# Kernel optimization log

Measured on AMD Instinct MI355X. Metric: run time of the kernel, lower is better.

Reference implementation:

```python
import jax, jax.numpy as jnp
import numpy as np

KSIZE, STRIDES, D_NEURON, DK, DV, NH, DACT, FINAL_DIM = 4, 2, 128, 128, 256, 8, 8, 256
N = KSIZE * KSIZE          # 16 neurons per window
DKH = DK // NH             # 16 == N (required by broadcast in original code)
DVH = DV // NH             # 32


def setup_inputs() -> dict:
    key = jax.random.key(0)
    ks = jax.random.split(key, 12)
    B, H, W, C = 32, 64, 64, 256
    def dense(kw, kb, fan_in, fan_out):
        w = jax.random.normal(kw, (fan_in, fan_out), jnp.float32) / np.sqrt(fan_in)
        b = jnp.zeros((fan_out,), jnp.float32)
        return w, b
    inps = jax.random.normal(ks[0], (B, H, W, C), jnp.float32)
    neuron_emb = jax.random.normal(ks[1], (KSIZE, KSIZE, D_NEURON), jnp.float32) / np.sqrt(D_NEURON)
    wkq_w, wkq_b = dense(ks[2], ks[3], D_NEURON, 2 * DK)
    wv_w, wv_b = dense(ks[4], ks[5], C, DV)
    wgactq_w, wgactq_b = dense(ks[6], ks[7], D_NEURON, DACT)
    wgactk_w, wgactk_b = dense(ks[8], ks[9], C, DACT)
    wf_w, wf_b = dense(ks[10], ks[11], DV, FINAL_DIM)
    return dict(inps=inps, neuron_emb=neuron_emb, wkq_w=wkq_w, wkq_b=wkq_b,
                wv_w=wv_w, wv_b=wv_b, wgactq_w=wgactq_w, wgactq_b=wgactq_b,
                wgactk_w=wgactk_w, wgactk_b=wgactk_b, wf_w=wf_w, wf_b=wf_b)


def _forward(inps, neuron_emb, wkq_w, wkq_b, wv_w, wv_b,
             wgactq_w, wgactq_b, wgactk_w, wgactk_b, wf_w, wf_b):
    B, H, W, C = inps.shape
    # ---- neural structures (tiny, per-head n x n softmax) ----
    kq = neuron_emb @ wkq_w + wkq_b                      # (k,k,2dk)
    k_part, q_part = jnp.split(kq, 2, axis=-1)           # each (k,k,dk)
    flat = lambda t: t.reshape(N, NH, DKH).transpose(1, 0, 2)   # (Nh,n,dkh)
    fk, fq = flat(k_part), flat(q_part)
    # broadcast add requires dkh == n: logits[h,i,j] = fq[h,i,j] + fk[h,j,i]
    logits = fq + fk.transpose(0, 2, 1)                  # (Nh,n,n)
    structures = jax.nn.softmax(logits, axis=-1)
    s0 = structures[:, 0, :]                             # (Nh,n) row 0 per head
    # ---- activation amounts (dacth == 1, i.e. dact == Nh) ----
    actk = inps @ wgactk_w + wgactk_b                    # (B,H,W,Nh)
    actq = (neuron_emb @ wgactq_w + wgactq_b).reshape(N, NH)   # (n,Nh)
    qv = actq[N - 2]                                     # slice [-2:-1] -> (Nh,)
    g = jax.nn.relu(qv[None, None, None, :] + actk)      # (B,H,W,Nh)
    denom = jnp.sum(g, axis=(1, 2), keepdims=True)       # (B,1,1,Nh)
    act = (float(H * W) / (denom + 1e-6)) * g            # (B,H,W,Nh)
    # ---- values, gated per head ----
    v = inps @ wv_w + wv_b                               # (B,H,W,dv)
    v = (v.reshape(B, H, W, NH, DVH) * act[..., None]).reshape(B, H, W, DV)
    # ---- SAME-padded im2col patches (TF extract_patches ordering kh,kw,c) ----
    nH, nW = -(-H // STRIDES), -(-W // STRIDES)
    pad_h = max((nH - 1) * STRIDES + KSIZE - H, 0)
    pad_w = max((nW - 1) * STRIDES + KSIZE - W, 0)
    vp = jnp.pad(v, ((0, 0), (pad_h // 2, pad_h - pad_h // 2),
                     (pad_w // 2, pad_w - pad_w // 2), (0, 0)))
    hi = (nH - 1) * STRIDES + 1
    wi = (nW - 1) * STRIDES + 1
    patches = jnp.stack([vp[:, i:i + hi:STRIDES, j:j + wi:STRIDES, :]
                         for i in range(KSIZE) for j in range(KSIZE)],
                        axis=3)                           # (B,nH,nW,n,dv)
    p = patches.reshape(B, nH, nW, N, NH, DVH)
    # weighted reduce over window positions with structure row 0
    out = jnp.einsum('hn,bxynhd->bxyhd', s0, p).reshape(B, nH, nW, DV)
    return out @ wf_w + wf_b                             # (B,nH,nW,final_dim)


def reference(inps, neuron_emb, wkq_w, wkq_b, wv_w, wv_b,
              wgactq_w, wgactq_b, wgactk_w, wgactk_b, wf_w, wf_b):
    return _forward(inps, neuron_emb, wkq_w, wkq_b, wv_w, wv_b,
                    wgactq_w, wgactq_b, wgactk_w, wgactk_b, wf_w, wf_b)
```

## Files before the change

### kernel.cpp

```cpp
#include <hip/hip_runtime.h>
#include <hip/hip_bf16.h>

#define B_    32
#define H_    64
#define W_    64
#define C_    256
#define NH_   8
#define N_    16
#define PIX_  (B_*H_*W_)
#define OUTPIX_ (B_*32*32)

typedef __hip_bfloat16 bf16;
typedef __attribute__((ext_vector_type(8))) short bf16x8;
typedef __attribute__((ext_vector_type(4))) float f32x4;

__device__ __forceinline__ float bf2f(unsigned short u) {
  union { unsigned int i; float f; } v; v.i = ((unsigned int)u) << 16; return v.f;
}
__device__ __forceinline__ unsigned pk2(float a, float b) {
  union { __hip_bfloat162 h2; unsigned u; } c;
  c.h2 = __float22bfloat162_rn(make_float2(a, b));
  return c.u;
}
__device__ __forceinline__ bf16x8 cvt8(float4 lo, float4 hi) {
  union { bf16x8 v; unsigned u[4]; } r;
  r.u[0] = pk2(lo.x, lo.y); r.u[1] = pk2(lo.z, lo.w);
  r.u[2] = pk2(hi.x, hi.y); r.u[3] = pk2(hi.z, hi.w);
  return r.v;
}

__global__ __launch_bounds__(256) void k1_setup(
    const float* __restrict__ emb, const float* __restrict__ wkq_w,
    const float* __restrict__ wkq_b, const float* __restrict__ wgq_w,
    const float* __restrict__ wgq_b,
    float* __restrict__ s0, float* __restrict__ qv) {
  __shared__ float lq[128];
  __shared__ float lk[16][8];
  int t = threadIdx.x;
  if (t < 128) {
    float acc = wkq_b[128 + t];
    for (int e = 0; e < 128; ++e) acc += emb[e] * wkq_w[e * 256 + 128 + t];
    lq[t] = acc;
  } else {
    int idx = t - 128; int j = idx >> 3, h = idx & 7;
    float acc = wkq_b[h * 16];
    for (int e = 0; e < 128; ++e) acc += emb[j * 128 + e] * wkq_w[e * 256 + h * 16];
    lk[j][h] = acc;
  }
  __syncthreads();
  if (t < 8) {
    float l[16]; float m = -1e30f;
    for (int j = 0; j < 16; ++j) { l[j] = lq[t * 16 + j] + lk[j][t]; m = fmaxf(m, l[j]); }
    float s = 0.f;
    for (int j = 0; j < 16; ++j) { l[j] = expf(l[j] - m); s += l[j]; }
    float inv = 1.f / s;
    for (int j = 0; j < 16; ++j) s0[t * 16 + j] = l[j] * inv;
    float acc = wgq_b[t];
    for (int e = 0; e < 128; ++e) acc += emb[14 * 128 + e] * wgq_w[e * 8 + t];
    qv[t] = acc;
  }
}

__global__ __launch_bounds__(256) void prep(
    const float* __restrict__ wv, const float* __restrict__ wf,
    const float* __restrict__ wgk,
    bf16* __restrict__ wvT, bf16* __restrict__ wfT, bf16* __restrict__ wgkT) {
  int bid = blockIdx.x, t = threadIdx.x;
  if (bid < 32) {
    __shared__ unsigned short tile[64][72];
    const float* src = (bid < 16) ? wv : wf;
    bf16* dst = (bid < 16) ? wvT : wfT;
    int tb = bid & 15, tr = tb >> 2, tc = tb & 3;
#pragma unroll
    for (int it = 0; it < 16; ++it) {
      int idx = it * 256 + t, row = idx >> 6, col = idx & 63;
      bf16 h = __float2bfloat16(src[(tr * 64 + row) * 256 + tc * 64 + col]);
      tile[row][col] = *(unsigned short*)&h;
    }
    __syncthreads();
#pragma unroll
    for (int it = 0; it < 16; ++it) {
      int idx = it * 256 + t, row = idx >> 6, col = idx & 63;
      dst[(tc * 64 + row) * 256 + (tr * 64 + col)] = *(bf16*)&tile[col][row];
    }
  } else {
    __shared__ float g[2048];
#pragma unroll
    for (int it = 0; it < 8; ++it) g[it * 256 + t] = wgk[it * 256 + t];
    __syncthreads();
#pragma unroll
    for (int it = 0; it < 16; ++it) {
      int idx = it * 256 + t, a = idx >> 8, k = idx & 255;
      float v = (a < 8) ? g[k * 8 + a] : 0.f;
      wgkT[a * 256 + k] = __float2bfloat16(v);
    }
  }
}

__global__ __launch_bounds__(512, 4) void kA(
    const float* __restrict__ inps, const bf16* __restrict__ wvT,
    const bf16* __restrict__ wgkT, const float* __restrict__ wv_b,
    const float* __restrict__ wgk_b, const float* __restrict__ qv,
    bf16* __restrict__ vraw, float* __restrict__ gbuf,
    float* __restrict__ denom) {
  __shared__ float sden[8];
  __shared__ float qvb_s[8];
  int t = threadIdx.x;
  long pix0 = (long)blockIdx.x * 64;
  if (t < 8) { sden[t] = 0.f; qvb_s[t] = qv[t] + wgk_b[t]; }
  __syncthreads();

  int wave = t >> 6, lane = t & 63;
  int mw = wave >> 2, nw = wave & 3;
  int m0 = mw * 32, n0 = nw * 64;
  int lm = lane & 15, q = lane >> 4;
  bool gatew = (nw == 0);

  f32x4 acc[2][4], accg[2];
#pragma unroll
  for (int mf = 0; mf < 2; ++mf) {
    accg[mf] = (f32x4){0.f, 0.f, 0.f, 0.f};
#pragma unroll
    for (int nf = 0; nf < 4; ++nf) acc[mf][nf] = (f32x4){0.f, 0.f, 0.f, 0.f};
  }
  const float4* ar0 = (const float4*)(inps + (pix0 + m0 + lm) * 256);
  const float4* ar1 = (const float4*)(inps + (pix0 + m0 + 16 + lm) * 256);
  const bf16* brow = wvT + (n0 + lm) * 256;
  const bf16* grow = wgkT + lm * 256;

#pragma unroll
  for (int ks = 0; ks < 8; ++ks) {
    int i0 = ks * 8 + q * 2;
    float4 a0lo = ar0[i0], a0hi = ar0[i0 + 1];
    float4 a1lo = ar1[i0], a1hi = ar1[i0 + 1];
    int kof = ks * 32 + q * 8;
    bf16x8 b0 = *(const bf16x8*)(brow + kof);
    bf16x8 b1 = *(const bf16x8*)(brow + 4096 + kof);
    bf16x8 b2 = *(const bf16x8*)(brow + 8192 + kof);
    bf16x8 b3 = *(const bf16x8*)(brow + 12288 + kof);
    bf16x8 a0 = cvt8(a0lo, a0hi);
    bf16x8 a1 = cvt8(a1lo, a1hi);
    acc[0][0] = __builtin_amdgcn_mfma_f32_16x16x32_bf16(a0, b0, acc[0][0], 0, 0, 0);
    acc[1][0] = __builtin_amdgcn_mfma_f32_16x16x32_bf16(a1, b0, acc[1][0], 0, 0, 0);
    acc[0][1] = __builtin_amdgcn_mfma_f32_16x16x32_bf16(a0, b1, acc[0][1], 0, 0, 0);
    acc[1][1] = __builtin_amdgcn_mfma_f32_16x16x32_bf16(a1, b1, acc[1][1], 0, 0, 0);
    acc[0][2] = __builtin_amdgcn_mfma_f32_16x16x32_bf16(a0, b2, acc[0][2], 0, 0, 0);
    acc[1][2] = __builtin_amdgcn_mfma_f32_16x16x32_bf16(a1, b2, acc[1][2], 0, 0, 0);
    acc[0][3] = __builtin_amdgcn_mfma_f32_16x16x32_bf16(a0, b3, acc[0][3], 0, 0, 0);
    acc[1][3] = __builtin_amdgcn_mfma_f32_16x16x32_bf16(a1, b3, acc[1][3], 0, 0, 0);
    if (gatew) {
      bf16x8 bg = *(const bf16x8*)(grow + kof);
      accg[0] = __builtin_amdgcn_mfma_f32_16x16x32_bf16(a0, bg, accg[0], 0, 0, 0);
      accg[1] = __builtin_amdgcn_mfma_f32_16x16x32_bf16(a1, bg, accg[1], 0, 0, 0);
    }
  }

#pragma unroll
  for (int nf = 0; nf < 4; ++nf) {
    int col = n0 + nf * 16 + lm;
    float wb = wv_b[col];
#pragma unroll
    for (int mf = 0; mf < 2; ++mf) {
#pragma unroll
      for (int r = 0; r < 4; ++r) {
        int rl = m0 + mf * 16 + q * 4 + r;
        vraw[(pix0 + rl) * 256 + col] = __float2bfloat16(acc[mf][nf][r] + wb);
      }
    }
  }

  if (gatew) {
    float part = 0.f;
    if (lm < 8) {
#pragma unroll
      for (int mf = 0; mf < 2; ++mf) {
#pragma unroll
        for (int r = 0; r < 4; ++r) {
          int rl = m0 + mf * 16 + q * 4 + r;
          float gg = fmaxf(qvb_s[lm] + accg[mf][r], 0.f);
          gbuf[(pix0 + rl) * 8 + lm] = gg;
          part += gg;
        }
      }
    }
    part += __shfl_xor(part, 16, 64);
    part += __shfl_xor(part, 32, 64);
    if (lane < 16 && lm < 8) atomicAdd(&sden[lm], part);
  }
  __syncthreads();
  if (t < 8) atomicAdd(&denom[(int)(pix0 >> 12) * 8 + t], sden[t]);
}

__global__ __launch_bounds__(256) void kB(
    const bf16* __restrict__ vraw, const float* __restrict__ s0,
    const float* __restrict__ gbuf, const float* __restrict__ denom,
    const bf16* __restrict__ wfT, const float* __restrict__ wf_b,
    float* __restrict__ out) {
  __shared__ float scfsh[4][64][8];
  __shared__ __align__(16) unsigned short opsh[32][264];
  int t = threadIdx.x;
  int bx = blockIdx.x, b = bx >> 5, x = bx & 31;

  {
    int i = t >> 6, c = t & 63;
    int r = 2 * x + i - 1;
    if (r >= 0 && r < 64) {
      long p = (long)b * 4096 + r * 64 + c;
#pragma unroll
      for (int a = 0; a < 8; ++a)
        scfsh[i][c][a] = 4096.0f / (denom[b * 8 + a] + 1e-6f) * gbuf[p * 8 + a];
    } else {
#pragma unroll
      for (int a = 0; a < 8; ++a) scfsh[i][c][a] = 0.f;
    }
  }
  __syncthreads();

  int c2 = t & 127, yg = t >> 7;
  int h = c2 >> 4;
  float s0r[16];
#pragma unroll
  for (int n = 0; n < 16; ++n) s0r[n] = s0[h * 16 + n];
  const bf16* vsb = vraw + (long)b * (4096 * 256);
  for (int yi = 0; yi < 16; ++yi) {
    int y = yi * 2 + yg;
    float p0 = 0.f, p1 = 0.f;
#pragma unroll
    for (int i = 0; i < 4; ++i) {
      int r = 2 * x + i - 1;
      if (r < 0 || r >= 64) continue;
      const bf16* rowp = vsb + (long)r * 64 * 256 + 2 * c2;
#pragma unroll
      for (int j = 0; j < 4; ++j) {
        int c = 2 * y + j - 1;
        if (c < 0 || c >= 64) continue;
        float coef = s0r[i * 4 + j] * scfsh[i][c][h];
        unsigned u = *(const unsigned*)(rowp + (long)c * 256);
        p0 += coef * bf2f((unsigned short)(u & 0xffff));
        p1 += coef * bf2f((unsigned short)(u >> 16));
      }
    }
    *(unsigned*)&opsh[y][2 * c2] = pk2(p0, p1);
  }
  __syncthreads();

  int wave = t >> 6, lane = t & 63;
  int n0 = wave * 64;
  int lm = lane & 15, q = lane >> 4;
  f32x4 acc[2][4];
#pragma unroll
  for (int mf = 0; mf < 2; ++mf)
#pragma unroll
    for (int nf = 0; nf < 4; ++nf) acc[mf][nf] = (f32x4){0.f, 0.f, 0.f, 0.f};
  const bf16* brow = wfT + (n0 + lm) * 256;
#pragma unroll
  for (int ks = 0; ks < 8; ++ks) {
    int kof = ks * 32 + q * 8;
    bf16x8 a0 = *(const bf16x8*)(&opsh[lm][kof]);
    bf16x8 a1 = *(const bf16x8*)(&opsh[16 + lm][kof]);
#pragma unroll
    for (int nf = 0; nf < 4; ++nf) {
      bf16x8 bb = *(const bf16x8*)(brow + nf * 4096 + kof);
      acc[0][nf] = __builtin_amdgcn_mfma_f32_16x16x32_bf16(a0, bb, acc[0][nf], 0, 0, 0);
      acc[1][nf] = __builtin_amdgcn_mfma_f32_16x16x32_bf16(a1, bb, acc[1][nf], 0, 0, 0);
    }
  }
  long out0 = (long)bx * 32 * 256;
#pragma unroll
  for (int nf = 0; nf < 4; ++nf) {
    int col = n0 + nf * 16 + lm;
    float wb = wf_b[col];
#pragma unroll
    for (int mf = 0; mf < 2; ++mf) {
#pragma unroll
      for (int r = 0; r < 4; ++r) {
        int row = mf * 16 + q * 4 + r;
        out[out0 + row * 256 + col] = acc[mf][nf][r] + wb;
      }
    }
  }
}

extern "C" void kernel_launch(void* const* d_in, const int* in_sizes, int n_in,
                              void* d_out, int out_size, void* d_ws, size_t ws_size,
                              hipStream_t stream) {
  const float* inps  = (const float*)d_in[0];
  const float* emb   = (const float*)d_in[1];
  const float* wkq_w = (const float*)d_in[2];
  const float* wkq_b = (const float*)d_in[3];
  const float* wv_w  = (const float*)d_in[4];
  const float* wv_b  = (const float*)d_in[5];
  const float* wgq_w = (const float*)d_in[6];
  const float* wgq_b = (const float*)d_in[7];
  const float* wgk_w = (const float*)d_in[8];
  const float* wgk_b = (const float*)d_in[9];
  const float* wf_w  = (const float*)d_in[10];
  const float* wf_b  = (const float*)d_in[11];

  float* wsf   = (float*)d_ws;
  float* s0f   = wsf;
  float* qvf   = wsf + 128;
  float* denom = wsf + 256;
  float* gbuf  = wsf + 1024;
  bf16*  wvT   = (bf16*)(wsf + 1049600);
  bf16*  wfT   = (bf16*)(wsf + 1082368);
  bf16*  wgkT  = (bf16*)(wsf + 1115136);
  bf16*  vraw  = (bf16*)(wsf + 1117184);
  float* outp  = (float*)d_out;

  hipMemsetAsync((void*)denom, 0, 1024, stream);
  k1_setup<<<1, 256, 0, stream>>>(emb, wkq_w, wkq_b, wgq_w, wgq_b, s0f, qvf);
  prep<<<33, 256, 0, stream>>>(wv_w, wf_w, wgk_w, wvT, wfT, wgkT);
  kA<<<PIX_ / 64, 512, 0, stream>>>(inps, wvT, wgkT, wv_b, wgk_b, qvf,
                                    vraw, gbuf, denom);
  kB<<<OUTPIX_ / 32, 256, 0, stream>>>(vraw, s0f, gbuf, denom, wfT, wf_b, outp);
}
```

Measured before the change: 413.4 us.

## Stage input tile through LDS as bf16 with two-half prefetch in kA

Before this change, each of the four N-waves loaded the same fp32 input rows from global memory and converted them to bf16 on its own. Now the block loads the 64x256 input tile once with coalesced float4 reads, converts it to bf16, and stores it in a padded LDS buffer split into two K halves. The global load for the second half is issued before the first half is computed, so it overlaps the MFMAs. This removes the 4x redundant global reads and conversions, at the cost of about 34 KB of LDS per block, which could limit occupancy at 4 blocks per CU.

```diff
diff --git a/kernel.cpp b/kernel.cpp
--- a/kernel.cpp
+++ b/kernel.cpp
@@ -21,12 +21,6 @@
   union { __hip_bfloat162 h2; unsigned u; } c;
   c.h2 = __float22bfloat162_rn(make_float2(a, b));
   return c.u;
-}
-__device__ __forceinline__ bf16x8 cvt8(float4 lo, float4 hi) {
-  union { bf16x8 v; unsigned u[4]; } r;
-  r.u[0] = pk2(lo.x, lo.y); r.u[1] = pk2(lo.z, lo.w);
-  r.u[2] = pk2(hi.x, hi.y); r.u[3] = pk2(hi.z, hi.w);
-  return r.v;
 }
 
 __global__ __launch_bounds__(256) void k1_setup(
@@ -103,18 +97,44 @@
     const float* __restrict__ wgk_b, const float* __restrict__ qv,
     bf16* __restrict__ vraw, float* __restrict__ gbuf,
     float* __restrict__ denom) {
+  __shared__ __align__(16) unsigned short ldsA[2][64][136];
   __shared__ float sden[8];
   __shared__ float qvb_s[8];
   int t = threadIdx.x;
-  long pix0 = (long)blockIdx.x * 64;
+  const long pix0 = (long)blockIdx.x * 64;
   if (t < 8) { sden[t] = 0.f; qvb_s[t] = qv[t] + wgk_b[t]; }
-  __syncthreads();
 
   int wave = t >> 6, lane = t & 63;
   int mw = wave >> 2, nw = wave & 3;
   int m0 = mw * 32, n0 = nw * 64;
   int lm = lane & 15, q = lane >> 4;
   bool gatew = (nw == 0);
+  const bf16* brow = wvT + (n0 + lm) * 256;
+  const bf16* grow = wgkT + lm * 256;
+
+  int sr = t >> 5, sc4 = t & 31;
+  const float* sbase = inps + pix0 * 256 + sr * 256 + sc4 * 4;
+  float4 st[4];
+
+#define LOADH(h_)                                                            \
+  {                                                                          \
+    const float* s_ = sbase + (h_)*128;                                      \
+    _Pragma("unroll")                                                        \
+    for (int it = 0; it < 4; ++it)                                           \
+      st[it] = *(const float4*)(s_ + it * 16 * 256);                         \
+  }
+#define WRITEH(h_)                                                           \
+  {                                                                          \
+    _Pragma("unroll")                                                        \
+    for (int it = 0; it < 4; ++it)                                           \
+      *(uint2*)&ldsA[h_][it * 16 + sr][sc4 * 4] =                            \
+          make_uint2(pk2(st[it].x, st[it].y), pk2(st[it].z, st[it].w));      \
+  }
+
+  LOADH(0);
+  WRITEH(0);
+  LOADH(1);
+  __syncthreads();
 
   f32x4 acc[2][4], accg[2];
 #pragma unroll
@@ -123,37 +143,41 @@
 #pragma unroll
     for (int nf = 0; nf < 4; ++nf) acc[mf][nf] = (f32x4){0.f, 0.f, 0.f, 0.f};
   }
-  const float4* ar0 = (const float4*)(inps + (pix0 + m0 + lm) * 256);
-  const float4* ar1 = (const float4*)(inps + (pix0 + m0 + 16 + lm) * 256);
-  const bf16* brow = wvT + (n0 + lm) * 256;
-  const bf16* grow = wgkT + lm * 256;
-
-#pragma unroll
-  for (int ks = 0; ks < 8; ++ks) {
-    int i0 = ks * 8 + q * 2;
-    float4 a0lo = ar0[i0], a0hi = ar0[i0 + 1];
-    float4 a1lo = ar1[i0], a1hi = ar1[i0 + 1];
-    int kof = ks * 32 + q * 8;
-    bf16x8 b0 = *(const bf16x8*)(brow + kof);
-    bf16x8 b1 = *(const bf16x8*)(brow + 4096 + kof);
-    bf16x8 b2 = *(const bf16x8*)(brow + 8192 + kof);
-    bf16x8 b3 = *(const bf16x8*)(brow + 12288 + kof);
-    bf16x8 a0 = cvt8(a0lo, a0hi);
-    bf16x8 a1 = cvt8(a1lo, a1hi);
-    acc[0][0] = __builtin_amdgcn_mfma_f32_16x16x32_bf16(a0, b0, acc[0][0], 0, 0, 0);
-    acc[1][0] = __builtin_amdgcn_mfma_f32_16x16x32_bf16(a1, b0, acc[1][0], 0, 0, 0);
-    acc[0][1] = __builtin_amdgcn_mfma_f32_16x16x32_bf16(a0, b1, acc[0][1], 0, 0, 0);
-    acc[1][1] = __builtin_amdgcn_mfma_f32_16x16x32_bf16(a1, b1, acc[1][1], 0, 0, 0);
-    acc[0][2] = __builtin_amdgcn_mfma_f32_16x16x32_bf16(a0, b2, acc[0][2], 0, 0, 0);
-    acc[1][2] = __builtin_amdgcn_mfma_f32_16x16x32_bf16(a1, b2, acc[1][2], 0, 0, 0);
-    acc[0][3] = __builtin_amdgcn_mfma_f32_16x16x32_bf16(a0, b3, acc[0][3], 0, 0, 0);
-    acc[1][3] = __builtin_amdgcn_mfma_f32_16x16x32_bf16(a1, b3, acc[1][3], 0, 0, 0);
-    if (gatew) {
-      bf16x8 bg = *(const bf16x8*)(grow + kof);
-      accg[0] = __builtin_amdgcn_mfma_f32_16x16x32_bf16(a0, bg, accg[0], 0, 0, 0);
-      accg[1] = __builtin_amdgcn_mfma_f32_16x16x32_bf16(a1, bg, accg[1], 0, 0, 0);
-    }
-  }
+
+#define COMPUTEH(h_)                                                         \
+  {                                                                          \
+    const unsigned short* arow0 = &ldsA[h_][m0 + lm][0];                     \
+    const unsigned short* arow1 = &ldsA[h_][m0 + 16 + lm][0];                \
+    _Pragma("unroll")                                                        \
+    for (int ksl = 0; ksl < 4; ++ksl) {                                      \
+      int kof = ksl * 32 + q * 8;                                            \
+      bf16x8 a0 = *(const bf16x8*)(arow0 + kof);                             \
+      bf16x8 a1 = *(const bf16x8*)(arow1 + kof);                             \
+      int gk = (h_)*128 + kof;                                               \
+      bf16x8 b0 = *(const bf16x8*)(brow + gk);                               \
+      bf16x8 b1 = *(const bf16x8*)(brow + 4096 + gk);                        \
+      bf16x8 b2 = *(const bf16x8*)(brow + 8192 + gk);                        \
+      bf16x8 b3 = *(const bf16x8*)(brow + 12288 + gk);                       \
+      acc[0][0] = __builtin_amdgcn_mfma_f32_16x16x32_bf16(a0, b0, acc[0][0], 0, 0, 0); \
+      acc[1][0] = __builtin_amdgcn_mfma_f32_16x16x32_bf16(a1, b0, acc[1][0], 0, 0, 0); \
+      acc[0][1] = __builtin_amdgcn_mfma_f32_16x16x32_bf16(a0, b1, acc[0][1], 0, 0, 0); \
+      acc[1][1] = __builtin_amdgcn_mfma_f32_16x16x32_bf16(a1, b1, acc[1][1], 0, 0, 0); \
+      acc[0][2] = __builtin_amdgcn_mfma_f32_16x16x32_bf16(a0, b2, acc[0][2], 0, 0, 0); \
+      acc[1][2] = __builtin_amdgcn_mfma_f32_16x16x32_bf16(a1, b2, acc[1][2], 0, 0, 0); \
+      acc[0][3] = __builtin_amdgcn_mfma_f32_16x16x32_bf16(a0, b3, acc[0][3], 0, 0, 0); \
+      acc[1][3] = __builtin_amdgcn_mfma_f32_16x16x32_bf16(a1, b3, acc[1][3], 0, 0, 0); \
+      if (gatew) {                                                           \
+        bf16x8 bg = *(const bf16x8*)(grow + gk);                             \
+        accg[0] = __builtin_amdgcn_mfma_f32_16x16x32_bf16(a0, bg, accg[0], 0, 0, 0); \
+        accg[1] = __builtin_amdgcn_mfma_f32_16x16x32_bf16(a1, bg, accg[1], 0, 0, 0); \
+      }                                                                      \
+    }                                                                        \
+  }
+
+  COMPUTEH(0);
+  WRITEH(1);
+  __syncthreads();
+  COMPUTEH(1);
 
 #pragma unroll
   for (int nf = 0; nf < 4; ++nf) {
@@ -189,6 +213,9 @@
   }
   __syncthreads();
   if (t < 8) atomicAdd(&denom[(int)(pix0 >> 12) * 8 + t], sden[t]);
+#undef LOADH
+#undef WRITEH
+#undef COMPUTEH
 }
 
 __global__ __launch_bounds__(256) void kB(
```

After: 380.8 us. -7.9%, faster.
